# Performance work log

Measured on AMD Instinct MI355X. Metric: run time of the kernel, lower is better.

## Reference

```python
import jax, jax.numpy as jnp
import numpy as np

N = 8192
D_IN = 128
D_OUT = 128


def setup_inputs() -> dict:
    key = jax.random.key(0)
    k1, k2, k3 = jax.random.split(key, 3)
    node_features = jax.random.normal(k1, (N, D_IN), dtype=jnp.float32)
    adj_matrix = jax.random.uniform(k2, (N, N), dtype=jnp.float32)
    # Xavier-uniform weight, zero bias (as in reset_parameters)
    limit = float(np.sqrt(6.0 / (D_IN + D_OUT)))
    weight = jax.random.uniform(k3, (D_IN, D_OUT), dtype=jnp.float32,
                                minval=-limit, maxval=limit)
    bias = jnp.zeros((D_OUT,), dtype=jnp.float32)
    return {"node_features": node_features, "adj_matrix": adj_matrix,
            "weight": weight, "bias": bias}


def reference(node_features, adj_matrix, weight, bias):
    n = adj_matrix.shape[0]
    # A_hat = A + I
    a_hat = adj_matrix + jnp.eye(n, dtype=adj_matrix.dtype)
    d_hat = jnp.sum(a_hat, axis=1)  # [N]
    # pow(d, -0.5) with inf (d==0) masked to 0
    d_inv_sqrt = jnp.where(d_hat > 0, jax.lax.rsqrt(d_hat), 0.0)
    # diag(d) @ A_hat @ diag(d) == row/col broadcast scaling (same math)
    adj_normalized = d_inv_sqrt[:, None] * a_hat * d_inv_sqrt[None, :]
    support = node_features @ weight  # [N, D_OUT]
    out = adj_normalized @ support + bias
    return out
```

## Files before the change

### kernel.cpp

```cpp
#include <hip/hip_runtime.h>

#define NN 8192
#define DD 128

typedef short s16x4 __attribute__((ext_vector_type(4)));
typedef short s16x8 __attribute__((ext_vector_type(8)));
typedef float f32x4 __attribute__((ext_vector_type(4)));
typedef unsigned short u16;
typedef const void __attribute__((address_space(1))) gvoid;
typedef void __attribute__((address_space(3))) lvoid;

__device__ __forceinline__ u16 f2bf(float f) {
  unsigned int u = __float_as_uint(f);
  u += 0x7fffu + ((u >> 16) & 1u);
  return (u16)(u >> 16);
}
__device__ __forceinline__ float bf2f(u16 h) {
  return __uint_as_float(((unsigned int)h) << 16);
}

__global__ __launch_bounds__(256) void k_prep(const float* __restrict__ A,
                                              float* __restrict__ dinv,
                                              u16* __restrict__ Abf) {
  const int row = blockIdx.x;
  const float4* Ar = (const float4*)(A + (size_t)row * NN);
  ushort4* Br = (ushort4*)(Abf + (size_t)row * NN);
  const int t = threadIdx.x;
  float s = 0.f;
#pragma unroll
  for (int i = 0; i < 8; ++i) {
    float4 v = Ar[t + 256 * i];
    s += (v.x + v.y) + (v.z + v.w);
    ushort4 b;
    b.x = f2bf(v.x); b.y = f2bf(v.y); b.z = f2bf(v.z); b.w = f2bf(v.w);
    Br[t + 256 * i] = b;
  }
#pragma unroll
  for (int off = 32; off > 0; off >>= 1) s += __shfl_down(s, off, 64);
  __shared__ float red[4];
  if ((t & 63) == 0) red[t >> 6] = s;
  __syncthreads();
  if (t == 0) {
    float d = 1.0f + ((red[0] + red[1]) + (red[2] + red[3]));
    dinv[row] = d > 0.f ? rsqrtf(d) : 0.f;
  }
}

__global__ __launch_bounds__(256) void k_support(const float* __restrict__ X,
                                                 const float* __restrict__ W,
                                                 const float* __restrict__ dinv,
                                                 u16* __restrict__ tT) {
  __shared__ __align__(16) u16 Wt[128][136];
  __shared__ __align__(16) u16 Xs[32][136];
  const int t = threadIdx.x;
  const int j0 = blockIdx.x * 32;

  const float4* W4 = (const float4*)W;
#pragma unroll
  for (int s = 0; s < 16; ++s) {
    int c = t + 256 * s;
    int k = c >> 5, n4 = c & 31;
    float4 wv = W4[c];
    Wt[n4 * 4 + 0][k] = f2bf(wv.x);
    Wt[n4 * 4 + 1][k] = f2bf(wv.y);
    Wt[n4 * 4 + 2][k] = f2bf(wv.z);
    Wt[n4 * 4 + 3][k] = f2bf(wv.w);
  }
  const float4* X4 = (const float4*)(X + (size_t)j0 * DD);
#pragma unroll
  for (int s = 0; s < 4; ++s) {
    int c = t + 256 * s;
    int j = c >> 5, q = c & 31;
    float4 xv = X4[c];
    s16x4 p;
    p[0] = (short)f2bf(xv.x); p[1] = (short)f2bf(xv.y);
    p[2] = (short)f2bf(xv.z); p[3] = (short)f2bf(xv.w);
    *(s16x4*)&Xs[j][q * 4] = p;
  }
  __syncthreads();

  const int w = t >> 6, L = t & 63, lrow = L & 15, quad = L >> 4;
  f32x4 acc[2][2] = {};
#pragma unroll
  for (int ks = 0; ks < 4; ++ks) {
    const int k = ks * 32;
    s16x8 fa[2], fb[2];
#pragma unroll
    for (int nt = 0; nt < 2; ++nt)
      fa[nt] = *(const s16x8*)&Wt[w * 32 + nt * 16 + lrow][k + quad * 8];
#pragma unroll
    for (int jt = 0; jt < 2; ++jt)
      fb[jt] = *(const s16x8*)&Xs[jt * 16 + lrow][k + quad * 8];
#pragma unroll
    for (int nt = 0; nt < 2; ++nt)
#pragma unroll
      for (int jt = 0; jt < 2; ++jt)
        acc[nt][jt] = __builtin_amdgcn_mfma_f32_16x16x32_bf16(fa[nt], fb[jt], acc[nt][jt], 0, 0, 0);
  }

#pragma unroll
  for (int jt = 0; jt < 2; ++jt) {
    const int j = j0 + jt * 16 + lrow;
    const float dv = dinv[j];
#pragma unroll
    for (int nt = 0; nt < 2; ++nt) {
#pragma unroll
      for (int r = 0; r < 4; ++r) {
        const int n = w * 32 + nt * 16 + quad * 4 + r;
        tT[(size_t)n * NN + j] = f2bf(dv * acc[nt][jt][r]);
      }
    }
  }
}

#define TILE_BYTES 24576
__global__ __launch_bounds__(256) void k_gemm(const u16* __restrict__ Abf,
                                              const u16* __restrict__ tT,
                                              float* __restrict__ part) {
  __shared__ __align__(16) unsigned char sh[2][TILE_BYTES];
  const int t = threadIdx.x;
  const int bm = blockIdx.x >> 2;
  const int kq = blockIdx.x & 3;
  const int kbase = kq * (NN / 4);
  const int w = t >> 6, L = t & 63, lrow = L & 15, quad = L >> 4;
  const size_t row0 = (size_t)bm * 64;

  auto prefetch = [&](int buf, int k0) {
#pragma unroll
    for (int j = 0; j < 6; ++j) {
      const int g = w * 6 + j;
      const int o = g * 1024 + L * 16;
      const u16* src;
      if (g < 8) {
        const int r = o >> 7, c = (o >> 4) & 7;
        src = Abf + (row0 + r) * NN + (k0 + ((c ^ (r & 7)) << 3));
      } else {
        const int o2 = o - 8192;
        const int r = o2 >> 7, c = (o2 >> 4) & 7;
        src = tT + (size_t)r * NN + (k0 + ((c ^ (r & 7)) << 3));
      }
      __builtin_amdgcn_global_load_lds((gvoid*)src,
                                       (lvoid*)&sh[buf][g * 1024], 16, 0, 0);
    }
  };

  f32x4 acc[4][2] = {};
  prefetch(0, kbase);
  __syncthreads();

  for (int it = 0; it < 32; ++it) {
    const int cur = it & 1;
    if (it < 31) prefetch(cur ^ 1, kbase + (it + 1) * 64);
    const unsigned char* Ab = &sh[cur][0];
    const unsigned char* Bb = &sh[cur][8192];
#pragma unroll
    for (int s = 0; s < 2; ++s) {
      const int cx = (((s * 4) | quad) ^ (lrow & 7)) << 4;
      s16x8 fb0 = *(const s16x8*)(Bb + (w * 32 + lrow) * 128 + cx);
      s16x8 fb1 = *(const s16x8*)(Bb + (w * 32 + 16 + lrow) * 128 + cx);
#pragma unroll
      for (int mt = 0; mt < 4; ++mt) {
        s16x8 fa = *(const s16x8*)(Ab + (mt * 16 + lrow) * 128 + cx);
        acc[mt][0] = __builtin_amdgcn_mfma_f32_16x16x32_bf16(fa, fb0, acc[mt][0], 0, 0, 0);
        acc[mt][1] = __builtin_amdgcn_mfma_f32_16x16x32_bf16(fa, fb1, acc[mt][1], 0, 0, 0);
      }
    }
    __syncthreads();
  }

  float* pbase = part + (size_t)kq * NN * DD;
#pragma unroll
  for (int mt = 0; mt < 4; ++mt) {
#pragma unroll
    for (int r = 0; r < 4; ++r) {
      const int i = (int)row0 + mt * 16 + quad * 4 + r;
#pragma unroll
      for (int nt = 0; nt < 2; ++nt) {
        const int n = w * 32 + nt * 16 + lrow;
        pbase[(size_t)i * DD + n] = acc[mt][nt][r];
      }
    }
  }
}

__global__ __launch_bounds__(256) void k_reduce(const float* __restrict__ part,
                                                const u16* __restrict__ tT,
                                                const float* __restrict__ dinv,
                                                const float* __restrict__ bias,
                                                float* __restrict__ out) {
  const int gid = blockIdx.x * 256 + threadIdx.x;
  const int i = gid >> 5;
  const int c = gid & 31;
  const size_t idx = (size_t)i * 32 + c;
  const float4 p0 = ((const float4*)part)[idx];
  const float4 p1 = ((const float4*)(part + (size_t)NN * DD))[idx];
  const float4 p2 = ((const float4*)(part + (size_t)2 * NN * DD))[idx];
  const float4 p3 = ((const float4*)(part + (size_t)3 * NN * DD))[idx];
  const float4 bb = ((const float4*)bias)[c];
  const float dv = dinv[i];
  const int n = c * 4;
  float4 o;
  o.x = dv * (((p0.x + p1.x) + (p2.x + p3.x)) + bf2f(tT[(size_t)(n + 0) * NN + i])) + bb.x;
  o.y = dv * (((p0.y + p1.y) + (p2.y + p3.y)) + bf2f(tT[(size_t)(n + 1) * NN + i])) + bb.y;
  o.z = dv * (((p0.z + p1.z) + (p2.z + p3.z)) + bf2f(tT[(size_t)(n + 2) * NN + i])) + bb.z;
  o.w = dv * (((p0.w + p1.w) + (p2.w + p3.w)) + bf2f(tT[(size_t)(n + 3) * NN + i])) + bb.w;
  ((float4*)out)[idx] = o;
}

extern "C" void kernel_launch(void* const* d_in, const int* in_sizes, int n_in,
                              void* d_out, int out_size, void* d_ws, size_t ws_size,
                              hipStream_t stream) {
  const float* X    = (const float*)d_in[0];
  const float* A    = (const float*)d_in[1];
  const float* W    = (const float*)d_in[2];
  const float* bias = (const float*)d_in[3];
  float* out = (float*)d_out;

  float* dinv = (float*)d_ws;
  u16*   tT   = (u16*)((char*)d_ws + 32768);
  float* part = (float*)((char*)d_ws + 32768 + 2097152);
  u16*   Abf  = (u16*)((char*)d_ws + 32768 + 2097152 + 16777216);

  hipLaunchKernelGGL(k_prep,    dim3(8192), dim3(256), 0, stream, A, dinv, Abf);
  hipLaunchKernelGGL(k_support, dim3(256),  dim3(256), 0, stream, X, W, dinv, tT);
  hipLaunchKernelGGL(k_gemm,    dim3(512),  dim3(256), 0, stream, Abf, tT, part);
  hipLaunchKernelGGL(k_reduce,  dim3(1024), dim3(256), 0, stream, part, tT, dinv, bias, out);
}
```

Measured before the change: 438.8 us.

## Enlarge GEMM row tile to 128 and split K eight ways

The main GEMM block now covers 128 rows instead of 64, with a 2x2 wave layout so each wave computes a 64x64 output tile. The K dimension is split eight ways instead of four, which keeps the grid at 512 blocks. The larger tile loads each bf16 tT chunk once per 128 rows, cutting how often it is read from global memory. The costs are twice the fp32 partial-sum buffer, more traffic in the reduce kernel, more registers and 64KB of LDS per block.

```diff
diff --git a/kernel.cpp b/kernel.cpp
--- a/kernel.cpp
+++ b/kernel.cpp
@@ -113,29 +113,29 @@
   }
 }
 
-#define TILE_BYTES 24576
-__global__ __launch_bounds__(256) void k_gemm(const u16* __restrict__ Abf,
-                                              const u16* __restrict__ tT,
-                                              float* __restrict__ part) {
-  __shared__ __align__(16) unsigned char sh[2][TILE_BYTES];
+__global__ __launch_bounds__(256, 2) void k_gemm(const u16* __restrict__ Abf,
+                                                 const u16* __restrict__ tT,
+                                                 float* __restrict__ part) {
+  __shared__ __align__(16) unsigned char sh[2][32768];
   const int t = threadIdx.x;
-  const int bm = blockIdx.x >> 2;
-  const int kq = blockIdx.x & 3;
-  const int kbase = kq * (NN / 4);
+  const int bm = blockIdx.x >> 3;
+  const int kq = blockIdx.x & 7;
+  const int kbase = kq * (NN / 8);
   const int w = t >> 6, L = t & 63, lrow = L & 15, quad = L >> 4;
-  const size_t row0 = (size_t)bm * 64;
+  const int wr = w >> 1, wc = w & 1;
+  const size_t row0 = (size_t)bm * 128;
 
   auto prefetch = [&](int buf, int k0) {
 #pragma unroll
-    for (int j = 0; j < 6; ++j) {
-      const int g = w * 6 + j;
+    for (int j = 0; j < 8; ++j) {
+      const int g = w * 8 + j;
       const int o = g * 1024 + L * 16;
       const u16* src;
-      if (g < 8) {
+      if (g < 16) {
         const int r = o >> 7, c = (o >> 4) & 7;
         src = Abf + (row0 + r) * NN + (k0 + ((c ^ (r & 7)) << 3));
       } else {
-        const int o2 = o - 8192;
+        const int o2 = o - 16384;
         const int r = o2 >> 7, c = (o2 >> 4) & 7;
         src = tT + (size_t)r * NN + (k0 + ((c ^ (r & 7)) << 3));
       }
@@ -144,25 +144,28 @@
     }
   };
 
-  f32x4 acc[4][2] = {};
+  f32x4 acc[4][4] = {};
   prefetch(0, kbase);
   __syncthreads();
 
-  for (int it = 0; it < 32; ++it) {
+  for (int it = 0; it < 16; ++it) {
     const int cur = it & 1;
-    if (it < 31) prefetch(cur ^ 1, kbase + (it + 1) * 64);
+    if (it < 15) prefetch(cur ^ 1, kbase + (it + 1) * 64);
     const unsigned char* Ab = &sh[cur][0];
-    const unsigned char* Bb = &sh[cur][8192];
+    const unsigned char* Bb = &sh[cur][16384];
 #pragma unroll
     for (int s = 0; s < 2; ++s) {
       const int cx = (((s * 4) | quad) ^ (lrow & 7)) << 4;
-      s16x8 fb0 = *(const s16x8*)(Bb + (w * 32 + lrow) * 128 + cx);
-      s16x8 fb1 = *(const s16x8*)(Bb + (w * 32 + 16 + lrow) * 128 + cx);
+      s16x8 fb[4];
+#pragma unroll
+      for (int nt = 0; nt < 4; ++nt)
+        fb[nt] = *(const s16x8*)(Bb + (wc * 64 + nt * 16 + lrow) * 128 + cx);
 #pragma unroll
       for (int mt = 0; mt < 4; ++mt) {
-        s16x8 fa = *(const s16x8*)(Ab + (mt * 16 + lrow) * 128 + cx);
-        acc[mt][0] = __builtin_amdgcn_mfma_f32_16x16x32_bf16(fa, fb0, acc[mt][0], 0, 0, 0);
-        acc[mt][1] = __builtin_amdgcn_mfma_f32_16x16x32_bf16(fa, fb1, acc[mt][1], 0, 0, 0);
+        s16x8 fa = *(const s16x8*)(Ab + (wr * 64 + mt * 16 + lrow) * 128 + cx);
+#pragma unroll
+        for (int nt = 0; nt < 4; ++nt)
+          acc[mt][nt] = __builtin_amdgcn_mfma_f32_16x16x32_bf16(fa, fb[nt], acc[mt][nt], 0, 0, 0);
       }
     }
     __syncthreads();
@@ -173,10 +176,10 @@
   for (int mt = 0; mt < 4; ++mt) {
 #pragma unroll
     for (int r = 0; r < 4; ++r) {
-      const int i = (int)row0 + mt * 16 + quad * 4 + r;
-#pragma unroll
-      for (int nt = 0; nt < 2; ++nt) {
-        const int n = w * 32 + nt * 16 + lrow;
+      const int i = (int)row0 + wr * 64 + mt * 16 + quad * 4 + r;
+#pragma unroll
+      for (int nt = 0; nt < 4; ++nt) {
+        const int n = wc * 64 + nt * 16 + lrow;
         pbase[(size_t)i * DD + n] = acc[mt][nt][r];
       }
     }
@@ -192,18 +195,23 @@
   const int i = gid >> 5;
   const int c = gid & 31;
   const size_t idx = (size_t)i * 32 + c;
-  const float4 p0 = ((const float4*)part)[idx];
-  const float4 p1 = ((const float4*)(part + (size_t)NN * DD))[idx];
-  const float4 p2 = ((const float4*)(part + (size_t)2 * NN * DD))[idx];
-  const float4 p3 = ((const float4*)(part + (size_t)3 * NN * DD))[idx];
+  float4 p[8];
+#pragma unroll
+  for (int q = 0; q < 8; ++q)
+    p[q] = ((const float4*)(part + (size_t)q * NN * DD))[idx];
+  float4 s;
+  s.x = ((p[0].x + p[1].x) + (p[2].x + p[3].x)) + ((p[4].x + p[5].x) + (p[6].x + p[7].x));
+  s.y = ((p[0].y + p[1].y) + (p[2].y + p[3].y)) + ((p[4].y + p[5].y) + (p[6].y + p[7].y));
+  s.z = ((p[0].z + p[1].z) + (p[2].z + p[3].z)) + ((p[4].z + p[5].z) + (p[6].z + p[7].z));
+  s.w = ((p[0].w + p[1].w) + (p[2].w + p[3].w)) + ((p[4].w + p[5].w) + (p[6].w + p[7].w));
   const float4 bb = ((const float4*)bias)[c];
   const float dv = dinv[i];
   const int n = c * 4;
   float4 o;
-  o.x = dv * (((p0.x + p1.x) + (p2.x + p3.x)) + bf2f(tT[(size_t)(n + 0) * NN + i])) + bb.x;
-  o.y = dv * (((p0.y + p1.y) + (p2.y + p3.y)) + bf2f(tT[(size_t)(n + 1) * NN + i])) + bb.y;
-  o.z = dv * (((p0.z + p1.z) + (p2.z + p3.z)) + bf2f(tT[(size_t)(n + 2) * NN + i])) + bb.z;
-  o.w = dv * (((p0.w + p1.w) + (p2.w + p3.w)) + bf2f(tT[(size_t)(n + 3) * NN + i])) + bb.w;
+  o.x = dv * (s.x + bf2f(tT[(size_t)(n + 0) * NN + i])) + bb.x;
+  o.y = dv * (s.y + bf2f(tT[(size_t)(n + 1) * NN + i])) + bb.y;
+  o.z = dv * (s.z + bf2f(tT[(size_t)(n + 2) * NN + i])) + bb.z;
+  o.w = dv * (s.w + bf2f(tT[(size_t)(n + 3) * NN + i])) + bb.w;
   ((float4*)out)[idx] = o;
 }
 
@@ -219,7 +227,7 @@
   float* dinv = (float*)d_ws;
   u16*   tT   = (u16*)((char*)d_ws + 32768);
   float* part = (float*)((char*)d_ws + 32768 + 2097152);
-  u16*   Abf  = (u16*)((char*)d_ws + 32768 + 2097152 + 16777216);
+  u16*   Abf  = (u16*)((char*)d_ws + 32768 + 2097152 + 33554432);
 
   hipLaunchKernelGGL(k_prep,    dim3(8192), dim3(256), 0, stream, A, dinv, Abf);
   hipLaunchKernelGGL(k_support, dim3(256),  dim3(256), 0, stream, X, W, dinv, tT);
```

Result: faster. 428.1 us (median of 2 runs) (-2.4%).
